# Optimization experiments

Hardware: AMD Instinct MI355X
Metric: run time of the kernel (lower is better)

The kernel has to match this reference:

```python
import jax, jax.numpy as jnp
import numpy as np
import math

B, N, D, H, PAIR = 4, 512, 512, 16, 64
DH = D // H

def setup_inputs() -> dict:
    key = jax.random.key(0)
    ks = jax.random.split(key, 8)
    x = jax.random.normal(ks[0], (B, N, D), dtype=jnp.float32)
    pair_bias = jax.random.normal(ks[1], (B, N, N, PAIR), dtype=jnp.float32)
    atom_mask = jax.random.randint(ks[2], (B, N), 0, 2).astype(jnp.bool_)
    s = 1.0 / math.sqrt(D)
    Wq = jax.random.normal(ks[3], (D, D), dtype=jnp.float32) * s
    Wk = jax.random.normal(ks[4], (D, D), dtype=jnp.float32) * s
    Wv = jax.random.normal(ks[5], (D, D), dtype=jnp.float32) * s
    Wo = jax.random.normal(ks[6], (D, D), dtype=jnp.float32) * s
    Wp = jax.random.normal(ks[7], (PAIR, H), dtype=jnp.float32) * (1.0 / math.sqrt(PAIR))
    return {"x": x, "pair_bias": pair_bias, "Wq": Wq, "Wk": Wk, "Wv": Wv,
            "Wo": Wo, "Wp": Wp, "atom_mask": atom_mask}

def reference(x, pair_bias, Wq, Wk, Wv, Wo, Wp, atom_mask):
    b, n, d = x.shape
    # projections -> [B, H, N, DH]
    q = (x @ Wq).reshape(b, n, H, DH).transpose(0, 2, 1, 3)
    k = (x @ Wk).reshape(b, n, H, DH).transpose(0, 2, 1, 3)
    v = (x @ Wv).reshape(b, n, H, DH).transpose(0, 2, 1, 3)
    scores = jnp.einsum('bhnd,bhmd->bhnm', q, k) / math.sqrt(DH)
    # pair bias projected to heads: [B, H, N, N]
    bias = jnp.einsum('bnmp,ph->bhnm', pair_bias, Wp)
    pair_mask = atom_mask[:, :, None] & atom_mask[:, None, :]        # [B, N, N]
    bias = jnp.where(pair_mask[:, None, :, :], bias, 0.0)
    scores = scores + bias
    # key masking with finite large negative, as in the original
    scores = jnp.where(atom_mask[:, None, None, :], scores, jnp.float32(-1e6))
    attn = jax.nn.softmax(scores, axis=-1)
    out = jnp.einsum('bhnm,bhmd->bhnd', attn, v)
    out = out.transpose(0, 2, 1, 3).reshape(b, n, d)
    final = out @ Wo
    final = jnp.where(atom_mask[:, :, None], final, 0.0)
    return (final, attn)
```

## Files before the change

kernel.cpp:

```cpp
#include <hip/hip_runtime.h>

typedef __attribute__((ext_vector_type(8))) short short8;
typedef __attribute__((ext_vector_type(4))) float f32x4;

#define NB 4
#define NN 512
#define ND 512
#define NH 16
#define NDH 32
#define NPAIR 64

static __device__ __forceinline__ float bf2f(unsigned short u) {
    union { unsigned int i; float f; } x; x.i = ((unsigned int)u) << 16; return x.f;
}
static __device__ __forceinline__ unsigned short f2bf(float f) {
    union { float f; unsigned int i; } x; x.f = f;
    unsigned int i = x.i;
    unsigned int r = (i + 0x7fffu + ((i >> 16) & 1u)) >> 16;
    return (unsigned short)r;
}
static __device__ __forceinline__ short8 cvt8(const float4 lo, const float4 hi) {
    short8 r;
    r[0] = (short)f2bf(lo.x); r[1] = (short)f2bf(lo.y);
    r[2] = (short)f2bf(lo.z); r[3] = (short)f2bf(lo.w);
    r[4] = (short)f2bf(hi.x); r[5] = (short)f2bf(hi.y);
    r[6] = (short)f2bf(hi.z); r[7] = (short)f2bf(hi.w);
    return r;
}

__global__ __launch_bounds__(256) void qkv_kernel(
    const float* __restrict__ x, const float* __restrict__ Wq,
    const float* __restrict__ Wk, const float* __restrict__ Wv,
    float* __restrict__ q_ws, float* __restrict__ k_ws, ushort* __restrict__ vT_ws)
{
    __shared__ float xs[8 * 512];
    const int tid = threadIdx.x;
    const int row0 = blockIdx.x * 8;
    const int which = blockIdx.y;
    const float* W = (which == 0) ? Wq : (which == 1) ? Wk : Wv;

    {
        const float4* xg = (const float4*)(x + row0 * 512);
        float4* s = (float4*)xs;
        #pragma unroll
        for (int i = 0; i < 4; ++i) s[tid + i * 256] = xg[tid + i * 256];
    }
    __syncthreads();

    const int c0 = tid * 2;
    float acc[8][2];
    #pragma unroll
    for (int r = 0; r < 8; ++r) { acc[r][0] = 0.f; acc[r][1] = 0.f; }

    for (int kk = 0; kk < 512; kk += 4) {
        float w[4][2];
        #pragma unroll
        for (int j = 0; j < 4; ++j) {
            const float2 u = *(const float2*)(W + (kk + j) * 512 + c0);
            w[j][0] = u.x; w[j][1] = u.y;
        }
        #pragma unroll
        for (int r = 0; r < 8; ++r) {
            const float4 xv = *(const float4*)(xs + r * 512 + kk);
            acc[r][0] = fmaf(xv.x, w[0][0], acc[r][0]);
            acc[r][1] = fmaf(xv.x, w[0][1], acc[r][1]);
            acc[r][0] = fmaf(xv.y, w[1][0], acc[r][0]);
            acc[r][1] = fmaf(xv.y, w[1][1], acc[r][1]);
            acc[r][0] = fmaf(xv.z, w[2][0], acc[r][0]);
            acc[r][1] = fmaf(xv.z, w[2][1], acc[r][1]);
            acc[r][0] = fmaf(xv.w, w[3][0], acc[r][0]);
            acc[r][1] = fmaf(xv.w, w[3][1], acc[r][1]);
        }
    }

    const int h = c0 >> 5, dh = c0 & 31;
    #pragma unroll
    for (int r = 0; r < 8; ++r) {
        int row = row0 + r, b = row >> 9, n = row & 511;
        if (which < 2) {
            float* dst = (which == 0 ? q_ws : k_ws) + (((b * 16 + h) * 512 + n) * 32 + dh);
            *(float2*)dst = make_float2(acc[r][0], acc[r][1]);
        } else {
            ushort* base = vT_ws + ((b * 16 + h) * 32 + dh) * 512 + n;
            base[0]   = f2bf(acc[r][0]);
            base[512] = f2bf(acc[r][1]);
        }
    }
}

__global__ __launch_bounds__(256) void bias_kernel(
    const float* __restrict__ pb, const float* __restrict__ Wp,
    ushort* __restrict__ bias_ws)
{
    const int tid = threadIdx.x;
    const int lane = tid & 63, wid = tid >> 6;
    const int col = lane & 15, quad = lane >> 4;

    short8 b0, b1;
    #pragma unroll
    for (int j = 0; j < 8; ++j) {
        b0[j] = (short)f2bf(Wp[(quad * 8 + j) * 16 + col]);
        b1[j] = (short)f2bf(Wp[(32 + quad * 8 + j) * 16 + col]);
    }

    const int gw = blockIdx.x * 4 + wid;
    #pragma unroll
    for (int i = 0; i < 8; ++i) {
        int tile = gw * 8 + i;
        int mt = tile & 31, n = (tile >> 5) & 511, b = tile >> 14;
        int m0 = mt * 16;
        const float* ap = pb + ((size_t)((b * 512 + n) * 512) + m0 + col) * 64 + quad * 8;
        short8 a0 = cvt8(*(const float4*)(ap),      *(const float4*)(ap + 4));
        short8 a1 = cvt8(*(const float4*)(ap + 32), *(const float4*)(ap + 36));
        f32x4 acc = {0.f, 0.f, 0.f, 0.f};
        acc = __builtin_amdgcn_mfma_f32_16x16x32_bf16(a0, b0, acc, 0, 0, 0);
        acc = __builtin_amdgcn_mfma_f32_16x16x32_bf16(a1, b1, acc, 0, 0, 0);
        ushort4 o;
        o.x = f2bf(acc[0]); o.y = f2bf(acc[1]); o.z = f2bf(acc[2]); o.w = f2bf(acc[3]);
        *(ushort4*)(bias_ws + ((size_t)(b * 16 + col) * 512 + n) * 512 + m0 + quad * 4) = o;
    }
}

__global__ __launch_bounds__(256) void attn_av_kernel(
    const float* __restrict__ q_ws, const float* __restrict__ k_ws,
    const ushort* __restrict__ bias_ws, const ushort* __restrict__ vT,
    const int* __restrict__ am, float* __restrict__ attn,
    float* __restrict__ out_ws)
{
    __shared__ float qs[32 * 32];
    __shared__ int amq[32];
    __shared__ float wred[2][2][4];
    __shared__ float red[4 * 528];
    const int tid = threadIdx.x, lane = tid & 63, wid = tid >> 6;
    const int bh = blockIdx.x >> 4, nt = blockIdx.x & 15;
    const int b = bh >> 4, h = bh & 15;
    const int n0 = nt * 32;

    {
        const float4* qg = (const float4*)(q_ws + (size_t)(bh * 512 + n0) * 32);
        ((float4*)qs)[tid] = qg[tid];
    }
    if (tid < 32) amq[tid] = am[b * 512 + n0 + tid];

    float k0[32], k1[32];
    {
        const float4* kp  = (const float4*)(k_ws + (size_t)(bh * 512 + tid) * 32);
        const float4* kp2 = (const float4*)(k_ws + (size_t)(bh * 512 + tid + 256) * 32);
        #pragma unroll
        for (int j = 0; j < 8; ++j) {
            float4 u = kp[j];
            k0[j * 4 + 0] = u.x; k0[j * 4 + 1] = u.y; k0[j * 4 + 2] = u.z; k0[j * 4 + 3] = u.w;
            float4 u2 = kp2[j];
            k1[j * 4 + 0] = u2.x; k1[j * 4 + 1] = u2.y; k1[j * 4 + 2] = u2.z; k1[j * 4 + 3] = u2.w;
        }
    }
    const int km0 = am[b * 512 + tid];
    const int km1 = am[b * 512 + 256 + tid];
    __syncthreads();

    const float scale = 0.17677669529663687f;
    float* arow = attn + (size_t)(bh * 512 + n0) * 512;
    const ushort* brow = bias_ws + (size_t)(bh * 512 + n0) * 512;

    for (int r = 0; r < 32; ++r) {
        float s0 = 0.f, s1 = 0.f;
        const float4* q4 = (const float4*)(qs + r * 32);
        #pragma unroll
        for (int j = 0; j < 8; ++j) {
            float4 qv = q4[j];
            s0 = fmaf(qv.x, k0[j * 4 + 0], s0); s1 = fmaf(qv.x, k1[j * 4 + 0], s1);
            s0 = fmaf(qv.y, k0[j * 4 + 1], s0); s1 = fmaf(qv.y, k1[j * 4 + 1], s1);
            s0 = fmaf(qv.z, k0[j * 4 + 2], s0); s1 = fmaf(qv.z, k1[j * 4 + 2], s1);
            s0 = fmaf(qv.w, k0[j * 4 + 3], s0); s1 = fmaf(qv.w, k1[j * 4 + 3], s1);
        }
        float bias0 = bf2f(brow[r * 512 + tid]);
        float bias1 = bf2f(brow[r * 512 + tid + 256]);
        int rm = amq[r];
        s0 = s0 * scale + ((rm && km0) ? bias0 : 0.f);
        s1 = s1 * scale + ((rm && km1) ? bias1 : 0.f);
        if (!km0) s0 = -1e6f;
        if (!km1) s1 = -1e6f;

        const int par = r & 1;
        float mloc = fmaxf(s0, s1);
        #pragma unroll
        for (int off = 32; off > 0; off >>= 1) mloc = fmaxf(mloc, __shfl_xor(mloc, off));
        if (lane == 0) wred[par][0][wid] = mloc;
        __syncthreads();
        float mx = fmaxf(fmaxf(wred[par][0][0], wred[par][0][1]),
                         fmaxf(wred[par][0][2], wred[par][0][3]));
        float p0 = __expf(s0 - mx), p1 = __expf(s1 - mx);
        float sl = p0 + p1;
        #pragma unroll
        for (int off = 32; off > 0; off >>= 1) sl += __shfl_xor(sl, off);
        if (lane == 0) wred[par][1][wid] = sl;
        __syncthreads();
        float inv = 1.0f / (wred[par][1][0] + wred[par][1][1] +
                            wred[par][1][2] + wred[par][1][3]);
        arow[r * 512 + tid]       = p0 * inv;
        arow[r * 512 + tid + 256] = p1 * inv;
    }

    __syncthreads();
    const int col = lane & 15, quad = lane >> 4;
    const int t = wid & 1, kh = wid >> 1;

    const float*  ap  = attn + (size_t)(bh * 512 + n0 + t * 16 + col) * 512 + kh * 256 + quad * 8;
    const ushort* vp0 = vT + (size_t)(bh * 32 + col) * 512 + kh * 256 + quad * 8;
    const ushort* vp1 = vp0 + 16 * 512;

    f32x4 acc0 = {0.f, 0.f, 0.f, 0.f}, acc1 = {0.f, 0.f, 0.f, 0.f};
    #pragma unroll
    for (int kc = 0; kc < 8; ++kc) {
        int mo = kc * 32;
        short8 a  = cvt8(*(const float4*)(ap + mo), *(const float4*)(ap + mo + 4));
        short8 v0 = *(const short8*)(vp0 + mo);
        short8 v1 = *(const short8*)(vp1 + mo);
        acc0 = __builtin_amdgcn_mfma_f32_16x16x32_bf16(a, v0, acc0, 0, 0, 0);
        acc1 = __builtin_amdgcn_mfma_f32_16x16x32_bf16(a, v1, acc1, 0, 0, 0);
    }
    {
        float* my = red + wid * 528;
        #pragma unroll
        for (int r = 0; r < 4; ++r) {
            my[(quad * 4 + r) * 33 + col]      = acc0[r];
            my[(quad * 4 + r) * 33 + 16 + col] = acc1[r];
        }
    }
    __syncthreads();
    if (wid < 2) {
        const float* r0 = red + wid * 528;
        const float* r1 = red + (2 + wid) * 528;
        float* op = out_ws + (size_t)(b * 512 + n0 + wid * 16 + quad * 4) * 512 + h * 32;
        #pragma unroll
        for (int r = 0; r < 4; ++r) {
            int i0 = (quad * 4 + r) * 33 + col;
            op[r * 512 + col]      = r0[i0] + r1[i0];
            op[r * 512 + 16 + col] = r0[i0 + 16] + r1[i0 + 16];
        }
    }
}

__global__ __launch_bounds__(256) void out_kernel(
    const float* __restrict__ out_in, const float* __restrict__ Wo,
    const int* __restrict__ am, float* __restrict__ fin)
{
    __shared__ float xs[8 * 512];
    const int tid = threadIdx.x;
    const int row0 = blockIdx.x * 8;
    {
        const float4* g = (const float4*)(out_in + (size_t)row0 * 512);
        float4* s = (float4*)xs;
        #pragma unroll
        for (int i = 0; i < 4; ++i) s[tid + i * 256] = g[tid + i * 256];
    }
    __syncthreads();

    const int c0 = tid * 2;
    float acc[8][2];
    #pragma unroll
    for (int r = 0; r < 8; ++r) { acc[r][0] = 0.f; acc[r][1] = 0.f; }

    for (int kk = 0; kk < 512; kk += 4) {
        float w[4][2];
        #pragma unroll
        for (int j = 0; j < 4; ++j) {
            const float2 u = *(const float2*)(Wo + (kk + j) * 512 + c0);
            w[j][0] = u.x; w[j][1] = u.y;
        }
        #pragma unroll
        for (int r = 0; r < 8; ++r) {
            const float4 xv = *(const float4*)(xs + r * 512 + kk);
            acc[r][0] = fmaf(xv.x, w[0][0], acc[r][0]);
            acc[r][1] = fmaf(xv.x, w[0][1], acc[r][1]);
            acc[r][0] = fmaf(xv.y, w[1][0], acc[r][0]);
            acc[r][1] = fmaf(xv.y, w[1][1], acc[r][1]);
            acc[r][0] = fmaf(xv.z, w[2][0], acc[r][0]);
            acc[r][1] = fmaf(xv.z, w[2][1], acc[r][1]);
            acc[r][0] = fmaf(xv.w, w[3][0], acc[r][0]);
            acc[r][1] = fmaf(xv.w, w[3][1], acc[r][1]);
        }
    }
    #pragma unroll
    for (int r = 0; r < 8; ++r) {
        int row = row0 + r, b = row >> 9, n = row & 511;
        float msk = am[b * 512 + n] ? 1.0f : 0.0f;
        *(float2*)(fin + (size_t)row * 512 + c0) =
            make_float2(acc[r][0] * msk, acc[r][1] * msk);
    }
}

extern "C" void kernel_launch(void* const* d_in, const int* in_sizes, int n_in,
                              void* d_out, int out_size, void* d_ws, size_t ws_size,
                              hipStream_t stream)
{
    const float* x  = (const float*)d_in[0];
    const float* pb = (const float*)d_in[1];
    const float* Wq = (const float*)d_in[2];
    const float* Wk = (const float*)d_in[3];
    const float* Wv = (const float*)d_in[4];
    const float* Wo = (const float*)d_in[5];
    const float* Wp = (const float*)d_in[6];
    const int*   am = (const int*)d_in[7];

    float* fin  = (float*)d_out;
    float* attn = fin + (size_t)NB * NN * ND;

    float*  q_ws    = (float*)d_ws;
    float*  k_ws    = (float*)((char*)d_ws + 4u * 1024 * 1024);
    ushort* vT      = (ushort*)((char*)d_ws + 8u * 1024 * 1024);
    float*  out_ws  = (float*)((char*)d_ws + 10u * 1024 * 1024);
    ushort* bias_ws = (ushort*)((char*)d_ws + 14u * 1024 * 1024);

    hipLaunchKernelGGL(qkv_kernel, dim3(256, 3), dim3(256), 0, stream,
                       x, Wq, Wk, Wv, q_ws, k_ws, vT);
    hipLaunchKernelGGL(bias_kernel, dim3(2048), dim3(256), 0, stream,
                       pb, Wp, bias_ws);
    hipLaunchKernelGGL(attn_av_kernel, dim3(1024), dim3(256), 0, stream,
                       q_ws, k_ws, bias_ws, vT, am, attn, out_ws);
    hipLaunchKernelGGL(out_kernel, dim3(256), dim3(256), 0, stream,
                       out_ws, Wo, am, fin);
}
```

Baseline: 595.7 us.

## Move projections and attention scores to split-bf16 MFMA with per-wave softmax

Moves the QKV and output projections from scalar FP32 FMA loops onto bf16 MFMA. Precision is kept by splitting each value into hi and lo bf16 parts and summing three MFMA products, and a new prep kernel transposes and splits the weights and x. The attention kernel now computes QK^T with MFMA and does the softmax for 16 rows per wave in registers, replacing the per-row block-wide reductions and their __syncthreads. It also stages P in LDS for the PV MFMA instead of re-reading attn from global memory. The split arithmetic triples the MFMA count and adds workspace traffic and an extra launch, and the results may differ slightly from FP32.

```diff
diff --git a/kernel.cpp b/kernel.cpp
--- a/kernel.cpp
+++ b/kernel.cpp
@@ -28,62 +28,122 @@
     return r;
 }
 
-__global__ __launch_bounds__(256) void qkv_kernel(
+__global__ __launch_bounds__(256) void prep_kernel(
     const float* __restrict__ x, const float* __restrict__ Wq,
     const float* __restrict__ Wk, const float* __restrict__ Wv,
-    float* __restrict__ q_ws, float* __restrict__ k_ws, ushort* __restrict__ vT_ws)
-{
-    __shared__ float xs[8 * 512];
+    const float* __restrict__ Wo,
+    ushort* __restrict__ x_hi, ushort* __restrict__ x_lo,
+    ushort* __restrict__ wt_hi, ushort* __restrict__ wt_lo)
+{
     const int tid = threadIdx.x;
-    const int row0 = blockIdx.x * 8;
-    const int which = blockIdx.y;
-    const float* W = (which == 0) ? Wq : (which == 1) ? Wk : Wv;
-
-    {
-        const float4* xg = (const float4*)(x + row0 * 512);
-        float4* s = (float4*)xs;
+    const int bid = blockIdx.x;
+    if (bid < 256) {
+        __shared__ float ws_[64][65];
+        const int mi = bid >> 6;
+        const int t = bid & 63;
+        const int tr = t >> 3, tc = t & 7;
+        const float* W = (mi == 0) ? Wq : (mi == 1) ? Wk : (mi == 2) ? Wv : Wo;
         #pragma unroll
-        for (int i = 0; i < 4; ++i) s[tid + i * 256] = xg[tid + i * 256];
-    }
-    __syncthreads();
-
-    const int c0 = tid * 2;
-    float acc[8][2];
-    #pragma unroll
-    for (int r = 0; r < 8; ++r) { acc[r][0] = 0.f; acc[r][1] = 0.f; }
-
-    for (int kk = 0; kk < 512; kk += 4) {
-        float w[4][2];
+        for (int p = 0; p < 4; ++p) {
+            const int r = p * 16 + (tid >> 4);
+            const int c4 = tid & 15;
+            const float4 v = *(const float4*)(W + (size_t)(tr * 64 + r) * 512 + tc * 64 + c4 * 4);
+            ws_[r][c4 * 4 + 0] = v.x; ws_[r][c4 * 4 + 1] = v.y;
+            ws_[r][c4 * 4 + 2] = v.z; ws_[r][c4 * 4 + 3] = v.w;
+        }
+        __syncthreads();
+        ushort* oh = wt_hi + (size_t)mi * 512 * 512;
+        ushort* ol = wt_lo + (size_t)mi * 512 * 512;
         #pragma unroll
-        for (int j = 0; j < 4; ++j) {
-            const float2 u = *(const float2*)(W + (kk + j) * 512 + c0);
-            w[j][0] = u.x; w[j][1] = u.y;
-        }
+        for (int p = 0; p < 4; ++p) {
+            const int n = p * 16 + (tid >> 4);
+            const int c4 = tid & 15;
+            const float v0 = ws_[c4 * 4 + 0][n];
+            const float v1 = ws_[c4 * 4 + 1][n];
+            const float v2 = ws_[c4 * 4 + 2][n];
+            const float v3 = ws_[c4 * 4 + 3][n];
+            ushort4 h4, l4;
+            h4.x = f2bf(v0); l4.x = f2bf(v0 - bf2f(h4.x));
+            h4.y = f2bf(v1); l4.y = f2bf(v1 - bf2f(h4.y));
+            h4.z = f2bf(v2); l4.z = f2bf(v2 - bf2f(h4.z));
+            h4.w = f2bf(v3); l4.w = f2bf(v3 - bf2f(h4.w));
+            const size_t o = (size_t)(tc * 64 + n) * 512 + tr * 64 + c4 * 4;
+            *(ushort4*)(oh + o) = h4;
+            *(ushort4*)(ol + o) = l4;
+        }
+    } else {
+        const int b2 = bid - 256;
+        const float4* xg = (const float4*)x;
+        for (int i = b2 * 256 + tid; i < (2048 * 512 / 4); i += 64 * 256) {
+            const float4 v = xg[i];
+            ushort4 h4, l4;
+            h4.x = f2bf(v.x); l4.x = f2bf(v.x - bf2f(h4.x));
+            h4.y = f2bf(v.y); l4.y = f2bf(v.y - bf2f(h4.y));
+            h4.z = f2bf(v.z); l4.z = f2bf(v.z - bf2f(h4.z));
+            h4.w = f2bf(v.w); l4.w = f2bf(v.w - bf2f(h4.w));
+            *(ushort4*)(x_hi + (size_t)i * 4) = h4;
+            *(ushort4*)(x_lo + (size_t)i * 4) = l4;
+        }
+    }
+}
+
+__global__ __launch_bounds__(256) void qkv_mfma_kernel(
+    const ushort* __restrict__ x_hi, const ushort* __restrict__ x_lo,
+    const ushort* __restrict__ wt_hi, const ushort* __restrict__ wt_lo,
+    ushort* __restrict__ q_hi, ushort* __restrict__ q_lo,
+    ushort* __restrict__ k_hi, ushort* __restrict__ k_lo,
+    ushort* __restrict__ vT)
+{
+    const int tid = threadIdx.x, lane = tid & 63, wid = tid >> 6;
+    const int c = lane & 15, qd = lane >> 4;
+    const int which = blockIdx.z;
+    const int m0 = blockIdx.y * 64 + wid * 16;
+    const int n0 = blockIdx.x * 64;
+    const ushort* wh = wt_hi + (size_t)which * 512 * 512;
+    const ushort* wl = wt_lo + (size_t)which * 512 * 512;
+
+    f32x4 z = {0.f, 0.f, 0.f, 0.f};
+    f32x4 acc[4];
+    #pragma unroll
+    for (int nt = 0; nt < 4; ++nt) acc[nt] = z;
+
+    const int arow = m0 + c;
+    for (int kc = 0; kc < 512; kc += 32) {
+        const short8 ah = *(const short8*)(x_hi + (size_t)arow * 512 + kc + qd * 8);
+        const short8 al = *(const short8*)(x_lo + (size_t)arow * 512 + kc + qd * 8);
         #pragma unroll
-        for (int r = 0; r < 8; ++r) {
-            const float4 xv = *(const float4*)(xs + r * 512 + kk);
-            acc[r][0] = fmaf(xv.x, w[0][0], acc[r][0]);
-            acc[r][1] = fmaf(xv.x, w[0][1], acc[r][1]);
-            acc[r][0] = fmaf(xv.y, w[1][0], acc[r][0]);
-            acc[r][1] = fmaf(xv.y, w[1][1], acc[r][1]);
-            acc[r][0] = fmaf(xv.z, w[2][0], acc[r][0]);
-            acc[r][1] = fmaf(xv.z, w[2][1], acc[r][1]);
-            acc[r][0] = fmaf(xv.w, w[3][0], acc[r][0]);
-            acc[r][1] = fmaf(xv.w, w[3][1], acc[r][1]);
-        }
-    }
-
-    const int h = c0 >> 5, dh = c0 & 31;
-    #pragma unroll
-    for (int r = 0; r < 8; ++r) {
-        int row = row0 + r, b = row >> 9, n = row & 511;
-        if (which < 2) {
-            float* dst = (which == 0 ? q_ws : k_ws) + (((b * 16 + h) * 512 + n) * 32 + dh);
-            *(float2*)dst = make_float2(acc[r][0], acc[r][1]);
+        for (int nt = 0; nt < 4; ++nt) {
+            const int bn = n0 + nt * 16 + c;
+            const short8 bh = *(const short8*)(wh + (size_t)bn * 512 + kc + qd * 8);
+            const short8 bl = *(const short8*)(wl + (size_t)bn * 512 + kc + qd * 8);
+            acc[nt] = __builtin_amdgcn_mfma_f32_16x16x32_bf16(ah, bh, acc[nt], 0, 0, 0);
+            acc[nt] = __builtin_amdgcn_mfma_f32_16x16x32_bf16(ah, bl, acc[nt], 0, 0, 0);
+            acc[nt] = __builtin_amdgcn_mfma_f32_16x16x32_bf16(al, bh, acc[nt], 0, 0, 0);
+        }
+    }
+
+    const int bb = m0 >> 9;
+    const int nbase = (m0 & 511) + qd * 4;
+    #pragma unroll
+    for (int nt = 0; nt < 4; ++nt) {
+        const int col = n0 + nt * 16 + c;
+        const int h = col >> 5, dh = col & 31;
+        if (which == 2) {
+            ushort4 o;
+            o.x = f2bf(acc[nt][0]); o.y = f2bf(acc[nt][1]);
+            o.z = f2bf(acc[nt][2]); o.w = f2bf(acc[nt][3]);
+            *(ushort4*)(vT + ((size_t)(bb * 16 + h) * 32 + dh) * 512 + nbase) = o;
         } else {
-            ushort* base = vT_ws + ((b * 16 + h) * 32 + dh) * 512 + n;
-            base[0]   = f2bf(acc[r][0]);
-            base[512] = f2bf(acc[r][1]);
+            ushort* oh = (which == 0) ? q_hi : k_hi;
+            ushort* ol = (which == 0) ? q_lo : k_lo;
+            #pragma unroll
+            for (int r = 0; r < 4; ++r) {
+                const size_t ad = ((size_t)(bb * 16 + h) * 512 + nbase + r) * 32 + dh;
+                const float v = acc[nt][r];
+                const unsigned short hi = f2bf(v);
+                oh[ad] = hi;
+                ol[ad] = f2bf(v - bf2f(hi));
+            }
         }
     }
 }
@@ -121,172 +181,158 @@
     }
 }
 
-__global__ __launch_bounds__(256) void attn_av_kernel(
-    const float* __restrict__ q_ws, const float* __restrict__ k_ws,
+__global__ __launch_bounds__(128) void attn_mfma_kernel(
+    const ushort* __restrict__ q_hi, const ushort* __restrict__ q_lo,
+    const ushort* __restrict__ k_hi, const ushort* __restrict__ k_lo,
     const ushort* __restrict__ bias_ws, const ushort* __restrict__ vT,
     const int* __restrict__ am, float* __restrict__ attn,
     float* __restrict__ out_ws)
 {
-    __shared__ float qs[32 * 32];
-    __shared__ int amq[32];
-    __shared__ float wred[2][2][4];
-    __shared__ float red[4 * 528];
+    __shared__ __align__(16) ushort Pl[2][16 * 512];
     const int tid = threadIdx.x, lane = tid & 63, wid = tid >> 6;
-    const int bh = blockIdx.x >> 4, nt = blockIdx.x & 15;
+    const int c = lane & 15, qd = lane >> 4;
+    const int job = blockIdx.x * 2 + wid;
+    const int bh = job >> 5, nt = job & 31;
     const int b = bh >> 4, h = bh & 15;
-    const int n0 = nt * 32;
-
-    {
-        const float4* qg = (const float4*)(q_ws + (size_t)(bh * 512 + n0) * 32);
-        ((float4*)qs)[tid] = qg[tid];
-    }
-    if (tid < 32) amq[tid] = am[b * 512 + n0 + tid];
-
-    float k0[32], k1[32];
-    {
-        const float4* kp  = (const float4*)(k_ws + (size_t)(bh * 512 + tid) * 32);
-        const float4* kp2 = (const float4*)(k_ws + (size_t)(bh * 512 + tid + 256) * 32);
+    const int n0 = nt * 16;
+
+    const size_t qoff = ((size_t)bh * 512 + n0 + c) * 32 + qd * 8;
+    const short8 qbh = *(const short8*)(q_hi + qoff);
+    const short8 qbl = *(const short8*)(q_lo + qoff);
+    const int rm = am[b * 512 + n0 + c];
+    const float scale = 0.17677669529663687f;
+
+    const ushort* khb = k_hi + (size_t)bh * 512 * 32 + qd * 8;
+    const ushort* klb = k_lo + (size_t)bh * 512 * 32 + qd * 8;
+    const ushort* brow = bias_ws + ((size_t)bh * 512 + n0 + c) * 512 + qd * 4;
+    const int* amk = am + b * 512 + qd * 4;
+
+    f32x4 p[32];
+    #pragma unroll
+    for (int mt = 0; mt < 32; ++mt) {
+        const int m0 = mt * 16;
+        const short8 kfh = *(const short8*)(khb + (size_t)(m0 + c) * 32);
+        const short8 kfl = *(const short8*)(klb + (size_t)(m0 + c) * 32);
+        f32x4 a = {0.f, 0.f, 0.f, 0.f};
+        a = __builtin_amdgcn_mfma_f32_16x16x32_bf16(kfh, qbh, a, 0, 0, 0);
+        a = __builtin_amdgcn_mfma_f32_16x16x32_bf16(kfh, qbl, a, 0, 0, 0);
+        a = __builtin_amdgcn_mfma_f32_16x16x32_bf16(kfl, qbh, a, 0, 0, 0);
+        const int4    km = *(const int4*)(amk + m0);
+        const ushort4 bs = *(const ushort4*)(brow + m0);
+        f32x4 o;
+        o[0] = km.x ? (a[0] * scale + (rm ? bf2f(bs.x) : 0.f)) : -1e6f;
+        o[1] = km.y ? (a[1] * scale + (rm ? bf2f(bs.y) : 0.f)) : -1e6f;
+        o[2] = km.z ? (a[2] * scale + (rm ? bf2f(bs.z) : 0.f)) : -1e6f;
+        o[3] = km.w ? (a[3] * scale + (rm ? bf2f(bs.w) : 0.f)) : -1e6f;
+        p[mt] = o;
+    }
+
+    float mx = -3e38f;
+    #pragma unroll
+    for (int mt = 0; mt < 32; ++mt)
+        mx = fmaxf(mx, fmaxf(fmaxf(p[mt][0], p[mt][1]), fmaxf(p[mt][2], p[mt][3])));
+    mx = fmaxf(mx, __shfl_xor(mx, 16));
+    mx = fmaxf(mx, __shfl_xor(mx, 32));
+
+    float sum = 0.f;
+    #pragma unroll
+    for (int mt = 0; mt < 32; ++mt) {
+        f32x4 e;
+        e[0] = __expf(p[mt][0] - mx);
+        e[1] = __expf(p[mt][1] - mx);
+        e[2] = __expf(p[mt][2] - mx);
+        e[3] = __expf(p[mt][3] - mx);
+        sum += (e[0] + e[1]) + (e[2] + e[3]);
+        p[mt] = e;
+    }
+    sum += __shfl_xor(sum, 16);
+    sum += __shfl_xor(sum, 32);
+    const float inv = 1.0f / sum;
+
+    float* arow = attn + ((size_t)bh * 512 + n0 + c) * 512;
+    ushort* pl = &Pl[wid][0] + c * 512;
+    #pragma unroll
+    for (int mt = 0; mt < 32; ++mt) {
+        f32x4 o;
+        o[0] = p[mt][0] * inv; o[1] = p[mt][1] * inv;
+        o[2] = p[mt][2] * inv; o[3] = p[mt][3] * inv;
+        *(f32x4*)(arow + mt * 16 + qd * 4) = o;
+        ushort4 pb4;
+        pb4.x = f2bf(o[0]); pb4.y = f2bf(o[1]);
+        pb4.z = f2bf(o[2]); pb4.w = f2bf(o[3]);
+        *(ushort4*)(pl + mt * 16 + qd * 4) = pb4;
+    }
+
+    f32x4 oc0 = {0.f, 0.f, 0.f, 0.f}, oc1 = {0.f, 0.f, 0.f, 0.f};
+    const ushort* vrow = vT + (size_t)bh * 32 * 512 + qd * 8;
+    #pragma unroll
+    for (int mc = 0; mc < 16; ++mc) {
+        const int m0 = mc * 32;
+        const short8 pf = *(const short8*)(pl + m0 + qd * 8);
+        const short8 v0 = *(const short8*)(vrow + (size_t)c * 512 + m0);
+        const short8 v1 = *(const short8*)(vrow + (size_t)(c + 16) * 512 + m0);
+        oc0 = __builtin_amdgcn_mfma_f32_16x16x32_bf16(v0, pf, oc0, 0, 0, 0);
+        oc1 = __builtin_amdgcn_mfma_f32_16x16x32_bf16(v1, pf, oc1, 0, 0, 0);
+    }
+    float* op = out_ws + ((size_t)b * 512 + n0 + c) * 512 + h * 32 + qd * 4;
+    *(f32x4*)(op) = oc0;
+    *(f32x4*)(op + 16) = oc1;
+}
+
+__global__ __launch_bounds__(256) void out_mfma_kernel(
+    const float* __restrict__ out_in, const ushort* __restrict__ wt_hi,
+    const ushort* __restrict__ wt_lo, const int* __restrict__ am,
+    float* __restrict__ fin)
+{
+    const int tid = threadIdx.x, lane = tid & 63, wid = tid >> 6;
+    const int c = lane & 15, qd = lane >> 4;
+    const int m0 = blockIdx.y * 64 + wid * 16;
+    const int n0 = blockIdx.x * 64;
+    const ushort* wh = wt_hi + (size_t)3 * 512 * 512;
+    const ushort* wl = wt_lo + (size_t)3 * 512 * 512;
+
+    f32x4 z = {0.f, 0.f, 0.f, 0.f};
+    f32x4 acc[4];
+    #pragma unroll
+    for (int nt = 0; nt < 4; ++nt) acc[nt] = z;
+
+    const int arow = m0 + c;
+    for (int kc = 0; kc < 512; kc += 32) {
+        const float4 xa = *(const float4*)(out_in + (size_t)arow * 512 + kc + qd * 8);
+        const float4 xb = *(const float4*)(out_in + (size_t)arow * 512 + kc + qd * 8 + 4);
+        short8 ah, al;
+        {
+            const float vv[8] = {xa.x, xa.y, xa.z, xa.w, xb.x, xb.y, xb.z, xb.w};
+            #pragma unroll
+            for (int j = 0; j < 8; ++j) {
+                const unsigned short hi = f2bf(vv[j]);
+                ah[j] = (short)hi;
+                al[j] = (short)f2bf(vv[j] - bf2f(hi));
+            }
+        }
         #pragma unroll
-        for (int j = 0; j < 8; ++j) {
-            float4 u = kp[j];
-            k0[j * 4 + 0] = u.x; k0[j * 4 + 1] = u.y; k0[j * 4 + 2] = u.z; k0[j * 4 + 3] = u.w;
-            float4 u2 = kp2[j];
-            k1[j * 4 + 0] = u2.x; k1[j * 4 + 1] = u2.y; k1[j * 4 + 2] = u2.z; k1[j * 4 + 3] = u2.w;
-        }
-    }
-    const int km0 = am[b * 512 + tid];
-    const int km1 = am[b * 512 + 256 + tid];
-    __syncthreads();
-
-    const float scale = 0.17677669529663687f;
-    float* arow = attn + (size_t)(bh * 512 + n0) * 512;
-    const ushort* brow = bias_ws + (size_t)(bh * 512 + n0) * 512;
-
-    for (int r = 0; r < 32; ++r) {
-        float s0 = 0.f, s1 = 0.f;
-        const float4* q4 = (const float4*)(qs + r * 32);
-        #pragma unroll
-        for (int j = 0; j < 8; ++j) {
-            float4 qv = q4[j];
-            s0 = fmaf(qv.x, k0[j * 4 + 0], s0); s1 = fmaf(qv.x, k1[j * 4 + 0], s1);
-            s0 = fmaf(qv.y, k0[j * 4 + 1], s0); s1 = fmaf(qv.y, k1[j * 4 + 1], s1);
-            s0 = fmaf(qv.z, k0[j * 4 + 2], s0); s1 = fmaf(qv.z, k1[j * 4 + 2], s1);
-            s0 = fmaf(qv.w, k0[j * 4 + 3], s0); s1 = fmaf(qv.w, k1[j * 4 + 3], s1);
-        }
-        float bias0 = bf2f(brow[r * 512 + tid]);
-        float bias1 = bf2f(brow[r * 512 + tid + 256]);
-        int rm = amq[r];
-        s0 = s0 * scale + ((rm && km0) ? bias0 : 0.f);
-        s1 = s1 * scale + ((rm && km1) ? bias1 : 0.f);
-        if (!km0) s0 = -1e6f;
-        if (!km1) s1 = -1e6f;
-
-        const int par = r & 1;
-        float mloc = fmaxf(s0, s1);
-        #pragma unroll
-        for (int off = 32; off > 0; off >>= 1) mloc = fmaxf(mloc, __shfl_xor(mloc, off));
-        if (lane == 0) wred[par][0][wid] = mloc;
-        __syncthreads();
-        float mx = fmaxf(fmaxf(wred[par][0][0], wred[par][0][1]),
-                         fmaxf(wred[par][0][2], wred[par][0][3]));
-        float p0 = __expf(s0 - mx), p1 = __expf(s1 - mx);
-        float sl = p0 + p1;
-        #pragma unroll
-        for (int off = 32; off > 0; off >>= 1) sl += __shfl_xor(sl, off);
-        if (lane == 0) wred[par][1][wid] = sl;
-        __syncthreads();
-        float inv = 1.0f / (wred[par][1][0] + wred[par][1][1] +
-                            wred[par][1][2] + wred[par][1][3]);
-        arow[r * 512 + tid]       = p0 * inv;
-        arow[r * 512 + tid + 256] = p1 * inv;
-    }
-
-    __syncthreads();
-    const int col = lane & 15, quad = lane >> 4;
-    const int t = wid & 1, kh = wid >> 1;
-
-    const float*  ap  = attn + (size_t)(bh * 512 + n0 + t * 16 + col) * 512 + kh * 256 + quad * 8;
-    const ushort* vp0 = vT + (size_t)(bh * 32 + col) * 512 + kh * 256 + quad * 8;
-    const ushort* vp1 = vp0 + 16 * 512;
-
-    f32x4 acc0 = {0.f, 0.f, 0.f, 0.f}, acc1 = {0.f, 0.f, 0.f, 0.f};
-    #pragma unroll
-    for (int kc = 0; kc < 8; ++kc) {
-        int mo = kc * 32;
-        short8 a  = cvt8(*(const float4*)(ap + mo), *(const float4*)(ap + mo + 4));
-        short8 v0 = *(const short8*)(vp0 + mo);
-        short8 v1 = *(const short8*)(vp1 + mo);
-        acc0 = __builtin_amdgcn_mfma_f32_16x16x32_bf16(a, v0, acc0, 0, 0, 0);
-        acc1 = __builtin_amdgcn_mfma_f32_16x16x32_bf16(a, v1, acc1, 0, 0, 0);
-    }
-    {
-        float* my = red + wid * 528;
-        #pragma unroll
-        for (int r = 0; r < 4; ++r) {
-            my[(quad * 4 + r) * 33 + col]      = acc0[r];
-            my[(quad * 4 + r) * 33 + 16 + col] = acc1[r];
-        }
-    }
-    __syncthreads();
-    if (wid < 2) {
-        const float* r0 = red + wid * 528;
-        const float* r1 = red + (2 + wid) * 528;
-        float* op = out_ws + (size_t)(b * 512 + n0 + wid * 16 + quad * 4) * 512 + h * 32;
-        #pragma unroll
-        for (int r = 0; r < 4; ++r) {
-            int i0 = (quad * 4 + r) * 33 + col;
-            op[r * 512 + col]      = r0[i0] + r1[i0];
-            op[r * 512 + 16 + col] = r0[i0 + 16] + r1[i0 + 16];
-        }
-    }
-}
-
-__global__ __launch_bounds__(256) void out_kernel(
-    const float* __restrict__ out_in, const float* __restrict__ Wo,
-    const int* __restrict__ am, float* __restrict__ fin)
-{
-    __shared__ float xs[8 * 512];
-    const int tid = threadIdx.x;
-    const int row0 = blockIdx.x * 8;
-    {
-        const float4* g = (const float4*)(out_in + (size_t)row0 * 512);
-        float4* s = (float4*)xs;
-        #pragma unroll
-        for (int i = 0; i < 4; ++i) s[tid + i * 256] = g[tid + i * 256];
-    }
-    __syncthreads();
-
-    const int c0 = tid * 2;
-    float acc[8][2];
-    #pragma unroll
-    for (int r = 0; r < 8; ++r) { acc[r][0] = 0.f; acc[r][1] = 0.f; }
-
-    for (int kk = 0; kk < 512; kk += 4) {
-        float w[4][2];
-        #pragma unroll
-        for (int j = 0; j < 4; ++j) {
-            const float2 u = *(const float2*)(Wo + (kk + j) * 512 + c0);
-            w[j][0] = u.x; w[j][1] = u.y;
-        }
-        #pragma unroll
-        for (int r = 0; r < 8; ++r) {
-            const float4 xv = *(const float4*)(xs + r * 512 + kk);
-            acc[r][0] = fmaf(xv.x, w[0][0], acc[r][0]);
-            acc[r][1] = fmaf(xv.x, w[0][1], acc[r][1]);
-            acc[r][0] = fmaf(xv.y, w[1][0], acc[r][0]);
-            acc[r][1] = fmaf(xv.y, w[1][1], acc[r][1]);
-            acc[r][0] = fmaf(xv.z, w[2][0], acc[r][0]);
-            acc[r][1] = fmaf(xv.z, w[2][1], acc[r][1]);
-            acc[r][0] = fmaf(xv.w, w[3][0], acc[r][0]);
-            acc[r][1] = fmaf(xv.w, w[3][1], acc[r][1]);
-        }
-    }
-    #pragma unroll
-    for (int r = 0; r < 8; ++r) {
-        int row = row0 + r, b = row >> 9, n = row & 511;
-        float msk = am[b * 512 + n] ? 1.0f : 0.0f;
-        *(float2*)(fin + (size_t)row * 512 + c0) =
-            make_float2(acc[r][0] * msk, acc[r][1] * msk);
+        for (int nt = 0; nt < 4; ++nt) {
+            const int bn = n0 + nt * 16 + c;
+            const short8 bh = *(const short8*)(wh + (size_t)bn * 512 + kc + qd * 8);
+            const short8 bl = *(const short8*)(wl + (size_t)bn * 512 + kc + qd * 8);
+            acc[nt] = __builtin_amdgcn_mfma_f32_16x16x32_bf16(ah, bh, acc[nt], 0, 0, 0);
+            acc[nt] = __builtin_amdgcn_mfma_f32_16x16x32_bf16(ah, bl, acc[nt], 0, 0, 0);
+            acc[nt] = __builtin_amdgcn_mfma_f32_16x16x32_bf16(al, bh, acc[nt], 0, 0, 0);
+        }
+    }
+
+    const int4 mk = *(const int4*)(am + m0 + qd * 4);
+    const float f0 = mk.x ? 1.f : 0.f;
+    const float f1 = mk.y ? 1.f : 0.f;
+    const float f2 = mk.z ? 1.f : 0.f;
+    const float f3 = mk.w ? 1.f : 0.f;
+    #pragma unroll
+    for (int nt = 0; nt < 4; ++nt) {
+        const size_t o = (size_t)(m0 + qd * 4) * 512 + n0 + nt * 16 + c;
+        fin[o]        = acc[nt][0] * f0;
+        fin[o + 512]  = acc[nt][1] * f1;
+        fin[o + 1024] = acc[nt][2] * f2;
+        fin[o + 1536] = acc[nt][3] * f3;
     }
 }
 
@@ -306,18 +352,27 @@
     float* fin  = (float*)d_out;
     float* attn = fin + (size_t)NB * NN * ND;
 
-    float*  q_ws    = (float*)d_ws;
-    float*  k_ws    = (float*)((char*)d_ws + 4u * 1024 * 1024);
-    ushort* vT      = (ushort*)((char*)d_ws + 8u * 1024 * 1024);
-    float*  out_ws  = (float*)((char*)d_ws + 10u * 1024 * 1024);
-    ushort* bias_ws = (ushort*)((char*)d_ws + 14u * 1024 * 1024);
-
-    hipLaunchKernelGGL(qkv_kernel, dim3(256, 3), dim3(256), 0, stream,
-                       x, Wq, Wk, Wv, q_ws, k_ws, vT);
+    char* ws = (char*)d_ws;
+    ushort* x_hi    = (ushort*)(ws);
+    ushort* x_lo    = (ushort*)(ws + 2u  * 1024 * 1024);
+    ushort* wt_hi   = (ushort*)(ws + 4u  * 1024 * 1024);
+    ushort* wt_lo   = (ushort*)(ws + 6u  * 1024 * 1024);
+    ushort* q_hi    = (ushort*)(ws + 8u  * 1024 * 1024);
+    ushort* q_lo    = (ushort*)(ws + 10u * 1024 * 1024);
+    ushort* k_hi    = (ushort*)(ws + 12u * 1024 * 1024);
+    ushort* k_lo    = (ushort*)(ws + 14u * 1024 * 1024);
+    ushort* vT      = (ushort*)(ws + 16u * 1024 * 1024);
+    float*  out_ws  = (float*) (ws + 18u * 1024 * 1024);
+    ushort* bias_ws = (ushort*)(ws + 22u * 1024 * 1024);
+
+    hipLaunchKernelGGL(prep_kernel, dim3(320), dim3(256), 0, stream,
+                       x, Wq, Wk, Wv, Wo, x_hi, x_lo, wt_hi, wt_lo);
     hipLaunchKernelGGL(bias_kernel, dim3(2048), dim3(256), 0, stream,
                        pb, Wp, bias_ws);
-    hipLaunchKernelGGL(attn_av_kernel, dim3(1024), dim3(256), 0, stream,
-                       q_ws, k_ws, bias_ws, vT, am, attn, out_ws);
-    hipLaunchKernelGGL(out_kernel, dim3(256), dim3(256), 0, stream,
-                       out_ws, Wo, am, fin);
-}
+    hipLaunchKernelGGL(qkv_mfma_kernel, dim3(8, 32, 3), dim3(256), 0, stream,
+                       x_hi, x_lo, wt_hi, wt_lo, q_hi, q_lo, k_hi, k_lo, vT);
+    hipLaunchKernelGGL(attn_mfma_kernel, dim3(1024), dim3(128), 0, stream,
+                       q_hi, q_lo, k_hi, k_lo, bias_ws, vT, am, attn, out_ws);
+    hipLaunchKernelGGL(out_mfma_kernel, dim3(8, 32), dim3(256), 0, stream,
+                       out_ws, wt_hi, wt_lo, am, fin);
+}
```

After: 543.4 us. 8.8% less time.
